# Optimization experiments

Measured on AMD Instinct MI355X. Metric: run time of the kernel, lower is better.

The kernel has to match this reference:

```python
import jax, jax.numpy as jnp
import numpy as np

N, E = 50000, 800000
IN, OUT, H, B = 512, 512, 8, 4  # num_bases=4, aggregators=['symnorm'] (PyG EGConv defaults)
FH = OUT // H  # per-head dim = 64
EPS = 1e-5


def setup_inputs() -> dict:
    key = jax.random.key(0)
    ks = jax.random.split(key, 8)
    s_in = 1.0 / np.sqrt(IN)
    return {
        "x": jax.random.normal(ks[0], (N, IN), jnp.float32),
        "edge_index": jax.random.randint(ks[1], (2, E), 0, N, jnp.int32),
        "W_bases": jax.random.normal(ks[2], (IN, B * FH), jnp.float32) * s_in,  # bases_lin (no bias)
        "W_comb": jax.random.normal(ks[3], (IN, H * B), jnp.float32) * s_in,    # comb_lin weight
        "b_comb": jnp.zeros((H * B,), jnp.float32),                               # comb_lin bias
        "conv_bias": jnp.zeros((OUT,), jnp.float32),                              # EGConv output bias
        "W_res": jax.random.normal(ks[4], (IN, OUT), jnp.float32) * s_in,        # res_connection
        "b_res": jnp.zeros((OUT,), jnp.float32),
        "gamma": jnp.ones((OUT,), jnp.float32),                                   # LayerNorm weight
        "beta": jnp.zeros((OUT,), jnp.float32),                                   # LayerNorm bias
    }


def reference(x, edge_index, W_bases, W_comb, b_comb, conv_bias, W_res, b_res, gamma, beta):
    n = x.shape[0]
    # --- gcn_norm with self-loops (symnorm aggregator) ---
    loops = jnp.arange(n, dtype=edge_index.dtype)
    src = jnp.concatenate([edge_index[0], loops])  # [E+N]
    dst = jnp.concatenate([edge_index[1], loops])
    deg = jax.ops.segment_sum(jnp.ones_like(src, dtype=x.dtype), dst, num_segments=n)
    dinv = jnp.where(deg > 0, jax.lax.rsqrt(jnp.maximum(deg, 1.0)), 0.0)
    norm = dinv[src] * dinv[dst]  # [E+N]

    # --- EGConv: bases projection, symnorm aggregation, per-head combination ---
    bases = x @ W_bases  # [N, B*FH]
    agg = jax.ops.segment_sum(bases[src] * norm[:, None], dst, num_segments=n)  # [N, B*FH]
    weightings = (x @ W_comb + b_comb).reshape(n, H, B)        # [N, H, B]  (num_aggrs=1)
    agg = agg.reshape(n, B, FH)                                  # [N, B, FH]
    conv_out = jnp.einsum('nhb,nbf->nhf', weightings, agg).reshape(n, OUT) + conv_bias

    # --- residual + LayerNorm + ReLU (dropout p=0 -> identity) ---
    out = conv_out + x @ W_res + b_res
    mu = out.mean(-1, keepdims=True)
    var = out.var(-1, keepdims=True)
    out = (out - mu) * jax.lax.rsqrt(var + EPS) * gamma + beta
    return jax.nn.relu(out)
```

## Files before the change

kernel.cpp:

```cpp
#include <hip/hip_runtime.h>
#include <hip/hip_bf16.h>

#define KDIM 512
#define ODIM 512
#define NB 4
#define NH 8
#define FH 64
#define BFH 256
#define HB 32
#define NCAT 896
#define COL_W 256
#define COL_R 288
#define LN_EPS 1e-5f
#define SCAN_BLK 1024

typedef __attribute__((ext_vector_type(8))) short short8;
typedef __attribute__((ext_vector_type(4))) float floatx4;

__device__ __forceinline__ float b2f(unsigned short u) {
    union { unsigned int i; float f; } v; v.i = ((unsigned int)u) << 16; return v.f;
}
__device__ __forceinline__ unsigned short f2b(float f) {
    __hip_bfloat16 h = __float2bfloat16(f);
    return *(unsigned short*)&h;
}
__device__ __forceinline__ void async16(const void* g, void* l) {
    __builtin_amdgcn_global_load_lds(
        (__attribute__((address_space(1))) unsigned int*)(g),
        (__attribute__((address_space(3))) unsigned int*)(l),
        16, 0, 0);
}

__global__ void deg_kernel(const int* __restrict__ dst, int* __restrict__ deg, int E) {
    int i = blockIdx.x * blockDim.x + threadIdx.x;
    if (i < E) atomicAdd(&deg[dst[i]], 1);
}

__global__ __launch_bounds__(256) void scan_sums_kernel(
        const int* __restrict__ deg, int* __restrict__ sums, int N) {
    int t = threadIdx.x;
    int idx = blockIdx.x * SCAN_BLK + t * 4;
    int4 v = {0, 0, 0, 0};
    if (idx + 3 < N) v = *(const int4*)(deg + idx);
    else {
        if (idx < N)     v.x = deg[idx];
        if (idx + 1 < N) v.y = deg[idx + 1];
        if (idx + 2 < N) v.z = deg[idx + 2];
        if (idx + 3 < N) v.w = deg[idx + 3];
    }
    int s = v.x + v.y + v.z + v.w;
    #pragma unroll
    for (int o = 32; o > 0; o >>= 1) s += __shfl_down(s, o, 64);
    __shared__ int ws[4];
    int lane = t & 63, w = t >> 6;
    if (lane == 0) ws[w] = s;
    __syncthreads();
    if (t == 0) sums[blockIdx.x] = ws[0] + ws[1] + ws[2] + ws[3];
}

__global__ __launch_bounds__(1024) void scan_base_kernel(
        int* __restrict__ sums, int nb) {
    __shared__ int sm[1024];
    int t = threadIdx.x;
    int own = (t < nb) ? sums[t] : 0;
    sm[t] = own;
    __syncthreads();
    for (int o = 1; o < 1024; o <<= 1) {
        int u = (t >= o) ? sm[t - o] : 0;
        __syncthreads();
        sm[t] += u;
        __syncthreads();
    }
    if (t < nb) sums[t] = sm[t] - own;
}

__global__ __launch_bounds__(256) void scan_write_kernel(
        const int* __restrict__ deg, const int* __restrict__ bases,
        int* __restrict__ offsets, int* __restrict__ woff,
        float* __restrict__ dinv, int N, int E) {
    int t = threadIdx.x;
    int idx = blockIdx.x * SCAN_BLK + t * 4;
    int4 v = {0, 0, 0, 0};
    if (idx + 3 < N) v = *(const int4*)(deg + idx);
    else {
        if (idx < N)     v.x = deg[idx];
        if (idx + 1 < N) v.y = deg[idx + 1];
        if (idx + 2 < N) v.z = deg[idx + 2];
        if (idx + 3 < N) v.w = deg[idx + 3];
    }
    int s = v.x + v.y + v.z + v.w;
    __shared__ int sm[256];
    sm[t] = s;
    __syncthreads();
    for (int o = 1; o < 256; o <<= 1) {
        int u = (t >= o) ? sm[t - o] : 0;
        __syncthreads();
        sm[t] += u;
        __syncthreads();
    }
    int o0 = sm[t] - s + bases[blockIdx.x];
    int o1 = o0 + v.x, o2 = o1 + v.y, o3 = o2 + v.z;
    if (idx + 3 < N) {
        int4 ov = {o0, o1, o2, o3};
        *(int4*)(offsets + idx) = ov;
        *(int4*)(woff + idx) = ov;
        float4 dv = {rsqrtf((float)v.x + 1.0f), rsqrtf((float)v.y + 1.0f),
                     rsqrtf((float)v.z + 1.0f), rsqrtf((float)v.w + 1.0f)};
        *(float4*)(dinv + idx) = dv;
    } else {
        int oo[4] = {o0, o1, o2, o3};
        int vv[4] = {v.x, v.y, v.z, v.w};
        for (int j = 0; j < 4; j++) {
            if (idx + j < N) {
                offsets[idx + j] = oo[j];
                woff[idx + j] = oo[j];
                dinv[idx + j] = rsqrtf((float)vv[j] + 1.0f);
            }
        }
    }
    if (blockIdx.x == 0 && t == 0) offsets[N] = E;
}

__global__ void fill_kernel(const int* __restrict__ src, const int* __restrict__ dst,
                            int* __restrict__ woff, int* __restrict__ ebuf, int E) {
    int i = blockIdx.x * blockDim.x + threadIdx.x;
    if (i < E) {
        int pos = atomicAdd(&woff[dst[i]], 1);
        ebuf[pos] = src[i];
    }
}

__global__ __launch_bounds__(256) void prep_kernel(
        const float* __restrict__ x, unsigned short* __restrict__ xb, long total4,
        int nCvtBlocks,
        const float* __restrict__ Wb, const float* __restrict__ Wc,
        const float* __restrict__ Wr, const float* __restrict__ bcomb,
        const float* __restrict__ bres,
        unsigned short* __restrict__ wT, float* __restrict__ bias_cat) {
    int blk = blockIdx.x;
    if (blk < nCvtBlocks) {
        long i = (long)blk * 256 + threadIdx.x;
        if (i >= total4) return;
        float4 v = ((const float4*)x)[i];
        ushort4 u;
        u.x = f2b(v.x); u.y = f2b(v.y); u.z = f2b(v.z); u.w = f2b(v.w);
        ((ushort4*)xb)[i] = u;
    } else {
        int idx = (blk - nCvtBlocks) * 256 + threadIdx.x;
        if (idx >= NCAT * KDIM) return;
        int c = idx >> 9, k = idx & (KDIM - 1);
        float v;
        if (c < BFH)                   v = Wb[(size_t)k * BFH + c];
        else if (c < COL_R)            v = Wc[(size_t)k * HB + (c - COL_W)];
        else if (c < COL_R + ODIM)     v = Wr[(size_t)k * ODIM + (c - COL_R)];
        else                           v = 0.0f;
        wT[(size_t)c * KDIM + k] = f2b(v);
        if (k == 0) {
            float bv = 0.0f;
            if (c >= COL_W && c < COL_R)             bv = bcomb[c - COL_W];
            else if (c >= COL_R && c < COL_R + ODIM) bv = bres[c - COL_R];
            bias_cat[c] = bv;
        }
    }
}

#define BM 128
#define BN 128
#define BK 32
#define SLD 136

__global__ __launch_bounds__(256) void mfma_gemm_kernel(
        const unsigned short* __restrict__ xb,
        const unsigned short* __restrict__ wT,
        const float* __restrict__ bias_cat,
        unsigned short* __restrict__ Cb,
        int N) {
    __shared__ short lds[16384];
    short* As0 = lds;
    short* Bs0 = lds + 4096;
    short* As1 = lds + 8192;
    short* Bs1 = lds + 12288;
    int t = threadIdx.x;
    int l = t & 63, w = t >> 6;
    int wr = w >> 1, wc = w & 1;
    int quad = l >> 4, m = l & 15;

    int nwg = gridDim.x;
    int orig = blockIdx.x;
    int q = nwg >> 3, r = nwg & 7;
    int xcd = orig & 7, slot = orig >> 3;
    int wg = (xcd < r) ? (xcd * (q + 1) + slot)
                       : (r * (q + 1) + (xcd - r) * q + slot);
    int bx = wg % 7, by = wg / 7;
    int row0 = by * BM;
    int col0 = bx * BN;

    floatx4 acc[4][4];
    floatx4 zero4 = {0.f, 0.f, 0.f, 0.f};
    #pragma unroll
    for (int i = 0; i < 4; i++)
        #pragma unroll
        for (int j = 0; j < 4; j++) acc[i][j] = zero4;

    int ar0 = row0 + (w << 4) + (l >> 2);
    int ar1 = ar0 + 64;
    int brow = col0 + (w << 4) + (l >> 2);
    int kk = (l & 3) * 8;
    const unsigned short* agp0 = xb + (size_t)min(ar0, N - 1) * KDIM + kk;
    const unsigned short* agp1 = xb + (size_t)min(ar1, N - 1) * KDIM + kk;
    const unsigned short* bgp0 = wT + (size_t)brow * KDIM + kk;
    const unsigned short* bgp1 = bgp0 + (size_t)64 * KDIM;

    auto stage = [&](short* A, short* B, int k0) {
        async16(agp0 + k0, A + w * 512);
        async16(agp1 + k0, A + 2048 + w * 512);
        async16(bgp0 + k0, B + w * 512);
        async16(bgp1 + k0, B + 2048 + w * 512);
    };
    auto compute = [&](const short* As, const short* Bs) {
        short8 a[4], b[4];
        #pragma unroll
        for (int i = 0; i < 4; i++)
            a[i] = *(const short8*)(As + (wr * 64 + i * 16 + m) * BK + quad * 8);
        #pragma unroll
        for (int j = 0; j < 4; j++)
            b[j] = *(const short8*)(Bs + (wc * 64 + j * 16 + m) * BK + quad * 8);
        #pragma unroll
        for (int i = 0; i < 4; i++)
            #pragma unroll
            for (int j = 0; j < 4; j++)
                acc[i][j] = __builtin_amdgcn_mfma_f32_16x16x32_bf16(
                    a[i], b[j], acc[i][j], 0, 0, 0);
    };

    stage(As0, Bs0, 0);
    __syncthreads();

    for (int k0 = 0; k0 < KDIM; k0 += 2 * BK) {
        if (k0 + BK < KDIM) stage(As1, Bs1, k0 + BK);
        compute(As0, Bs0);
        __syncthreads();
        if (k0 + 2 * BK < KDIM) stage(As0, Bs0, k0 + 2 * BK);
        compute(As1, Bs1);
        __syncthreads();
    }

    float bj[4];
    #pragma unroll
    for (int j = 0; j < 4; j++) bj[j] = bias_cat[col0 + wc * 64 + j * 16 + m];

    unsigned short* stage_buf = (unsigned short*)lds;
    #pragma unroll
    for (int i = 0; i < 4; i++) {
        __syncthreads();
        #pragma unroll
        for (int j = 0; j < 4; j++)
            #pragma unroll
            for (int r2 = 0; r2 < 4; r2++)
                stage_buf[(wr * 16 + quad * 4 + r2) * SLD + wc * 64 + j * 16 + m] =
                    f2b(acc[i][j][r2] + bj[j]);
        __syncthreads();
        #pragma unroll
        for (int u = t; u < 512; u += 256) {
            int lr = u >> 4, c8 = u & 15;
            int gr = row0 + ((lr & 16) ? 64 : 0) + i * 16 + (lr & 15);
            if (gr < N) {
                int4 v = *(const int4*)(stage_buf + lr * SLD + c8 * 8);
                *(int4*)(Cb + (size_t)gr * NCAT + col0 + c8 * 8) = v;
            }
        }
    }
}

__global__ __launch_bounds__(256) void gather_combine_kernel(
        const int* __restrict__ offsets, const int* __restrict__ ebuf,
        const float* __restrict__ dinv, const unsigned short* __restrict__ Cb,
        const float* __restrict__ conv_bias, const float* __restrict__ gamma,
        const float* __restrict__ beta, float* __restrict__ out, int N) {
    __shared__ float sagg[4][BFH];
    int wave = (blockIdx.x * blockDim.x + threadIdx.x) >> 6;
    int lane = threadIdx.x & 63;
    int wib = (threadIdx.x >> 6);
    if (wave >= N) return;
    int n = wave;
    float di = dinv[n];
    float self = di * di;
    ushort4 u = ((const ushort4*)(Cb + (size_t)n * NCAT))[lane];
    float ax = b2f(u.x) * self, ay = b2f(u.y) * self;
    float az = b2f(u.z) * self, aw = b2f(u.w) * self;
    int e = offsets[n], end = offsets[n + 1];
    int last = end - 1;
    for (; e < end; e += 8) {
        int s0, s1, s2, s3, s4, s5, s6, s7;
        float w0, w1, w2, w3, w4, w5, w6, w7;
        ushort4 u0, u1, u2, u3, u4, u5, u6, u7;
        s0 = ebuf[min(e + 0, last)];
        s1 = ebuf[min(e + 1, last)];
        s2 = ebuf[min(e + 2, last)];
        s3 = ebuf[min(e + 3, last)];
        s4 = ebuf[min(e + 4, last)];
        s5 = ebuf[min(e + 5, last)];
        s6 = ebuf[min(e + 6, last)];
        s7 = ebuf[min(e + 7, last)];
        w0 = (e + 0 < end) ? dinv[s0] * di : 0.0f;
        w1 = (e + 1 < end) ? dinv[s1] * di : 0.0f;
        w2 = (e + 2 < end) ? dinv[s2] * di : 0.0f;
        w3 = (e + 3 < end) ? dinv[s3] * di : 0.0f;
        w4 = (e + 4 < end) ? dinv[s4] * di : 0.0f;
        w5 = (e + 5 < end) ? dinv[s5] * di : 0.0f;
        w6 = (e + 6 < end) ? dinv[s6] * di : 0.0f;
        w7 = (e + 7 < end) ? dinv[s7] * di : 0.0f;
        u0 = ((const ushort4*)(Cb + (size_t)s0 * NCAT))[lane];
        u1 = ((const ushort4*)(Cb + (size_t)s1 * NCAT))[lane];
        u2 = ((const ushort4*)(Cb + (size_t)s2 * NCAT))[lane];
        u3 = ((const ushort4*)(Cb + (size_t)s3 * NCAT))[lane];
        u4 = ((const ushort4*)(Cb + (size_t)s4 * NCAT))[lane];
        u5 = ((const ushort4*)(Cb + (size_t)s5 * NCAT))[lane];
        u6 = ((const ushort4*)(Cb + (size_t)s6 * NCAT))[lane];
        u7 = ((const ushort4*)(Cb + (size_t)s7 * NCAT))[lane];
        ax += b2f(u0.x) * w0 + b2f(u1.x) * w1 + b2f(u2.x) * w2 + b2f(u3.x) * w3
            + b2f(u4.x) * w4 + b2f(u5.x) * w5 + b2f(u6.x) * w6 + b2f(u7.x) * w7;
        ay += b2f(u0.y) * w0 + b2f(u1.y) * w1 + b2f(u2.y) * w2 + b2f(u3.y) * w3
            + b2f(u4.y) * w4 + b2f(u5.y) * w5 + b2f(u6.y) * w6 + b2f(u7.y) * w7;
        az += b2f(u0.z) * w0 + b2f(u1.z) * w1 + b2f(u2.z) * w2 + b2f(u3.z) * w3
            + b2f(u4.z) * w4 + b2f(u5.z) * w5 + b2f(u6.z) * w6 + b2f(u7.z) * w7;
        aw += b2f(u0.w) * w0 + b2f(u1.w) * w1 + b2f(u2.w) * w2 + b2f(u3.w) * w3
            + b2f(u4.w) * w4 + b2f(u5.w) * w5 + b2f(u6.w) * w6 + b2f(u7.w) * w7;
    }
    float4 av = {ax, ay, az, aw};
    *(float4*)(&sagg[wib][lane * 4]) = av;

    int h = lane >> 3;
    int f0 = (lane & 7) * 8;
    int t0 = lane * 8;
    const unsigned short* crow = Cb + (size_t)n * NCAT;
    ushort4 wu = *(const ushort4*)(crow + COL_W + h * 4);
    float cw0 = b2f(wu.x), cw1 = b2f(wu.y), cw2 = b2f(wu.z), cw3 = b2f(wu.w);

    float4 b0a = *(const float4*)(&sagg[wib][0 * FH + f0]);
    float4 b0b = *(const float4*)(&sagg[wib][0 * FH + f0 + 4]);
    float4 b1a = *(const float4*)(&sagg[wib][1 * FH + f0]);
    float4 b1b = *(const float4*)(&sagg[wib][1 * FH + f0 + 4]);
    float4 b2a = *(const float4*)(&sagg[wib][2 * FH + f0]);
    float4 b2b = *(const float4*)(&sagg[wib][2 * FH + f0 + 4]);
    float4 b3a = *(const float4*)(&sagg[wib][3 * FH + f0]);
    float4 b3b = *(const float4*)(&sagg[wib][3 * FH + f0 + 4]);
    float a0[8] = {b0a.x, b0a.y, b0a.z, b0a.w, b0b.x, b0b.y, b0b.z, b0b.w};
    float a1[8] = {b1a.x, b1a.y, b1a.z, b1a.w, b1b.x, b1b.y, b1b.z, b1b.w};
    float a2[8] = {b2a.x, b2a.y, b2a.z, b2a.w, b2b.x, b2b.y, b2b.z, b2b.w};
    float a3[8] = {b3a.x, b3a.y, b3a.z, b3a.w, b3b.x, b3b.y, b3b.z, b3b.w};

    short8 rv = *(const short8*)(crow + COL_R + t0);
    float4 cb0 = *(const float4*)(conv_bias + t0);
    float4 cb1 = *(const float4*)(conv_bias + t0 + 4);
    float cb[8] = {cb0.x, cb0.y, cb0.z, cb0.w, cb1.x, cb1.y, cb1.z, cb1.w};

    float v[8];
    float s = 0.f, s2 = 0.f;
    #pragma unroll
    for (int j = 0; j < 8; j++) {
        float conv = cw0 * a0[j] + cw1 * a1[j] + cw2 * a2[j] + cw3 * a3[j];
        float val = conv + cb[j] + b2f((unsigned short)rv[j]);
        v[j] = val;
        s += val;
        s2 += val * val;
    }
    #pragma unroll
    for (int o = 32; o > 0; o >>= 1) {
        s  += __shfl_xor(s, o, 64);
        s2 += __shfl_xor(s2, o, 64);
    }
    float mu = s * (1.0f / (float)ODIM);
    float var = s2 * (1.0f / (float)ODIM) - mu * mu;
    float rstd = rsqrtf(var + LN_EPS);

    float4 g0 = *(const float4*)(gamma + t0);
    float4 g1 = *(const float4*)(gamma + t0 + 4);
    float4 be0 = *(const float4*)(beta + t0);
    float4 be1 = *(const float4*)(beta + t0 + 4);
    float g[8] = {g0.x, g0.y, g0.z, g0.w, g1.x, g1.y, g1.z, g1.w};
    float be[8] = {be0.x, be0.y, be0.z, be0.w, be1.x, be1.y, be1.z, be1.w};

    float ov[8];
    #pragma unroll
    for (int j = 0; j < 8; j++) {
        float o = (v[j] - mu) * rstd * g[j] + be[j];
        ov[j] = fmaxf(o, 0.0f);
    }
    float4* op = (float4*)(out + (size_t)n * ODIM + t0);
    op[0] = make_float4(ov[0], ov[1], ov[2], ov[3]);
    op[1] = make_float4(ov[4], ov[5], ov[6], ov[7]);
}

static inline char* ws_alloc(char*& p, size_t bytes) {
    char* r = p;
    p += (bytes + 255) & ~(size_t)255;
    return r;
}

extern "C" void kernel_launch(void* const* d_in, const int* in_sizes, int n_in,
                              void* d_out, int out_size, void* d_ws, size_t ws_size,
                              hipStream_t stream) {
    const float* x         = (const float*)d_in[0];
    const int*   ei        = (const int*)d_in[1];
    const float* W_bases   = (const float*)d_in[2];
    const float* W_comb    = (const float*)d_in[3];
    const float* b_comb    = (const float*)d_in[4];
    const float* conv_bias = (const float*)d_in[5];
    const float* W_res     = (const float*)d_in[6];
    const float* b_res     = (const float*)d_in[7];
    const float* gamma     = (const float*)d_in[8];
    const float* beta      = (const float*)d_in[9];

    int N = in_sizes[0] / KDIM;
    int E = in_sizes[1] / 2;
    const int* src = ei;
    const int* dst = ei + E;
    int nScanBlocks = (N + SCAN_BLK - 1) / SCAN_BLK;

    char* p = (char*)d_ws;
    int*   deg      = (int*)ws_alloc(p, sizeof(int) * (size_t)N);
    int*   offsets  = (int*)ws_alloc(p, sizeof(int) * (size_t)(N + 1));
    int*   woff     = (int*)ws_alloc(p, sizeof(int) * (size_t)N);
    int*   ebuf     = (int*)ws_alloc(p, sizeof(int) * (size_t)E);
    int*   sums     = (int*)ws_alloc(p, sizeof(int) * (size_t)nScanBlocks);
    float* dinv     = (float*)ws_alloc(p, sizeof(float) * (size_t)N);
    float* bias_cat = (float*)ws_alloc(p, sizeof(float) * NCAT);
    unsigned short* Cb  = (unsigned short*)ws_alloc(p, 2ull * N * NCAT);
    unsigned short* xb  = (unsigned short*)ws_alloc(p, 2ull * N * KDIM);
    unsigned short* wT  = (unsigned short*)ws_alloc(p, 2ull * NCAT * KDIM);
    float* out = (float*)d_out;

    hipMemsetAsync(deg, 0, sizeof(int) * (size_t)N, stream);

    long total4 = (long)N * KDIM / 4;
    int nCvtBlocks = (int)((total4 + 255) / 256);
    int nStageBlocks = (NCAT * KDIM + 255) / 256;
    prep_kernel<<<nCvtBlocks + nStageBlocks, 256, 0, stream>>>(
        x, xb, total4, nCvtBlocks, W_bases, W_comb, W_res, b_comb, b_res,
        wT, bias_cat);

    deg_kernel<<<(E + 255) / 256, 256, 0, stream>>>(dst, deg, E);
    scan_sums_kernel<<<nScanBlocks, 256, 0, stream>>>(deg, sums, N);
    scan_base_kernel<<<1, 1024, 0, stream>>>(sums, nScanBlocks);
    scan_write_kernel<<<nScanBlocks, 256, 0, stream>>>(deg, sums, offsets, woff,
                                                       dinv, N, E);
    fill_kernel<<<(E + 255) / 256, 256, 0, stream>>>(src, dst, woff, ebuf, E);

    int nYB = (N + BM - 1) / BM;
    mfma_gemm_kernel<<<7 * nYB, 256, 0, stream>>>(xb, wT, bias_cat, Cb, N);

    gather_combine_kernel<<<(N + 3) / 4, 256, 0, stream>>>(
        offsets, ebuf, dinv, Cb, conv_bias, gamma, beta, out, N);
}
```

Before: 423.5 us.

## Fuse degree count into prep, load GEMM B operand from global, split gather tail

The degree-counting atomics move into the prep kernel as extra blocks, which removes one kernel launch. The GEMM no longer stages the weight tile through LDS: each lane loads its B fragments straight from global memory, halving LDS use and dropping two async loads per stage. The gather loop gets an unclamped fast path for full groups of 8 edges and a separate masked tail. The direct global B loads are not shared across waves, which could raise L2 traffic and expose load latency inside the MFMA loop.

```diff
diff --git a/kernel.cpp b/kernel.cpp
--- a/kernel.cpp
+++ b/kernel.cpp
@@ -29,11 +29,6 @@
         (__attribute__((address_space(1))) unsigned int*)(g),
         (__attribute__((address_space(3))) unsigned int*)(l),
         16, 0, 0);
-}
-
-__global__ void deg_kernel(const int* __restrict__ dst, int* __restrict__ deg, int E) {
-    int i = blockIdx.x * blockDim.x + threadIdx.x;
-    if (i < E) atomicAdd(&deg[dst[i]], 1);
 }
 
 __global__ __launch_bounds__(256) void scan_sums_kernel(
@@ -132,11 +127,12 @@
 
 __global__ __launch_bounds__(256) void prep_kernel(
         const float* __restrict__ x, unsigned short* __restrict__ xb, long total4,
-        int nCvtBlocks,
+        int nCvtBlocks, int nStageBlocks,
         const float* __restrict__ Wb, const float* __restrict__ Wc,
         const float* __restrict__ Wr, const float* __restrict__ bcomb,
         const float* __restrict__ bres,
-        unsigned short* __restrict__ wT, float* __restrict__ bias_cat) {
+        unsigned short* __restrict__ wT, float* __restrict__ bias_cat,
+        const int* __restrict__ dst, int* __restrict__ deg, int E) {
     int blk = blockIdx.x;
     if (blk < nCvtBlocks) {
         long i = (long)blk * 256 + threadIdx.x;
@@ -145,7 +141,7 @@
         ushort4 u;
         u.x = f2b(v.x); u.y = f2b(v.y); u.z = f2b(v.z); u.w = f2b(v.w);
         ((ushort4*)xb)[i] = u;
-    } else {
+    } else if (blk < nCvtBlocks + nStageBlocks) {
         int idx = (blk - nCvtBlocks) * 256 + threadIdx.x;
         if (idx >= NCAT * KDIM) return;
         int c = idx >> 9, k = idx & (KDIM - 1);
@@ -161,6 +157,9 @@
             else if (c >= COL_R && c < COL_R + ODIM) bv = bres[c - COL_R];
             bias_cat[c] = bv;
         }
+    } else {
+        int i = (blk - nCvtBlocks - nStageBlocks) * 256 + threadIdx.x;
+        if (i < E) atomicAdd(&deg[dst[i]], 1);
     }
 }
 
@@ -175,11 +174,9 @@
         const float* __restrict__ bias_cat,
         unsigned short* __restrict__ Cb,
         int N) {
-    __shared__ short lds[16384];
+    __shared__ short lds[8192];
     short* As0 = lds;
-    short* Bs0 = lds + 4096;
-    short* As1 = lds + 8192;
-    short* Bs1 = lds + 12288;
+    short* As1 = lds + 4096;
     int t = threadIdx.x;
     int l = t & 63, w = t >> 6;
     int wr = w >> 1, wc = w & 1;
@@ -204,27 +201,26 @@
 
     int ar0 = row0 + (w << 4) + (l >> 2);
     int ar1 = ar0 + 64;
-    int brow = col0 + (w << 4) + (l >> 2);
     int kk = (l & 3) * 8;
     const unsigned short* agp0 = xb + (size_t)min(ar0, N - 1) * KDIM + kk;
     const unsigned short* agp1 = xb + (size_t)min(ar1, N - 1) * KDIM + kk;
-    const unsigned short* bgp0 = wT + (size_t)brow * KDIM + kk;
-    const unsigned short* bgp1 = bgp0 + (size_t)64 * KDIM;
-
-    auto stage = [&](short* A, short* B, int k0) {
+    const unsigned short* bq[4];
+    #pragma unroll
+    for (int j = 0; j < 4; j++)
+        bq[j] = wT + (size_t)(col0 + wc * 64 + j * 16 + m) * KDIM + quad * 8;
+
+    auto stage = [&](short* A, int k0) {
         async16(agp0 + k0, A + w * 512);
         async16(agp1 + k0, A + 2048 + w * 512);
-        async16(bgp0 + k0, B + w * 512);
-        async16(bgp1 + k0, B + 2048 + w * 512);
     };
-    auto compute = [&](const short* As, const short* Bs) {
+    auto compute = [&](const short* As, int k0) {
         short8 a[4], b[4];
+        #pragma unroll
+        for (int j = 0; j < 4; j++)
+            b[j] = *(const short8*)(bq[j] + k0);
         #pragma unroll
         for (int i = 0; i < 4; i++)
             a[i] = *(const short8*)(As + (wr * 64 + i * 16 + m) * BK + quad * 8);
-        #pragma unroll
-        for (int j = 0; j < 4; j++)
-            b[j] = *(const short8*)(Bs + (wc * 64 + j * 16 + m) * BK + quad * 8);
         #pragma unroll
         for (int i = 0; i < 4; i++)
             #pragma unroll
@@ -233,15 +229,15 @@
                     a[i], b[j], acc[i][j], 0, 0, 0);
     };
 
-    stage(As0, Bs0, 0);
+    stage(As0, 0);
     __syncthreads();
 
     for (int k0 = 0; k0 < KDIM; k0 += 2 * BK) {
-        if (k0 + BK < KDIM) stage(As1, Bs1, k0 + BK);
-        compute(As0, Bs0);
-        __syncthreads();
-        if (k0 + 2 * BK < KDIM) stage(As0, Bs0, k0 + 2 * BK);
-        compute(As1, Bs1);
+        if (k0 + BK < KDIM) stage(As1, k0 + BK);
+        compute(As0, k0);
+        __syncthreads();
+        if (k0 + 2 * BK < KDIM) stage(As0, k0 + 2 * BK);
+        compute(As1, k0 + BK);
         __syncthreads();
     }
 
@@ -289,35 +285,52 @@
     float ax = b2f(u.x) * self, ay = b2f(u.y) * self;
     float az = b2f(u.z) * self, aw = b2f(u.w) * self;
     int e = offsets[n], end = offsets[n + 1];
-    int last = end - 1;
-    for (; e < end; e += 8) {
-        int s0, s1, s2, s3, s4, s5, s6, s7;
-        float w0, w1, w2, w3, w4, w5, w6, w7;
-        ushort4 u0, u1, u2, u3, u4, u5, u6, u7;
-        s0 = ebuf[min(e + 0, last)];
-        s1 = ebuf[min(e + 1, last)];
-        s2 = ebuf[min(e + 2, last)];
-        s3 = ebuf[min(e + 3, last)];
-        s4 = ebuf[min(e + 4, last)];
-        s5 = ebuf[min(e + 5, last)];
-        s6 = ebuf[min(e + 6, last)];
-        s7 = ebuf[min(e + 7, last)];
-        w0 = (e + 0 < end) ? dinv[s0] * di : 0.0f;
-        w1 = (e + 1 < end) ? dinv[s1] * di : 0.0f;
-        w2 = (e + 2 < end) ? dinv[s2] * di : 0.0f;
-        w3 = (e + 3 < end) ? dinv[s3] * di : 0.0f;
-        w4 = (e + 4 < end) ? dinv[s4] * di : 0.0f;
-        w5 = (e + 5 < end) ? dinv[s5] * di : 0.0f;
-        w6 = (e + 6 < end) ? dinv[s6] * di : 0.0f;
-        w7 = (e + 7 < end) ? dinv[s7] * di : 0.0f;
-        u0 = ((const ushort4*)(Cb + (size_t)s0 * NCAT))[lane];
-        u1 = ((const ushort4*)(Cb + (size_t)s1 * NCAT))[lane];
-        u2 = ((const ushort4*)(Cb + (size_t)s2 * NCAT))[lane];
-        u3 = ((const ushort4*)(Cb + (size_t)s3 * NCAT))[lane];
-        u4 = ((const ushort4*)(Cb + (size_t)s4 * NCAT))[lane];
-        u5 = ((const ushort4*)(Cb + (size_t)s5 * NCAT))[lane];
-        u6 = ((const ushort4*)(Cb + (size_t)s6 * NCAT))[lane];
-        u7 = ((const ushort4*)(Cb + (size_t)s7 * NCAT))[lane];
+    for (; e + 8 <= end; e += 8) {
+        int s0 = ebuf[e + 0], s1 = ebuf[e + 1], s2 = ebuf[e + 2], s3 = ebuf[e + 3];
+        int s4 = ebuf[e + 4], s5 = ebuf[e + 5], s6 = ebuf[e + 6], s7 = ebuf[e + 7];
+        float w0 = dinv[s0] * di, w1 = dinv[s1] * di;
+        float w2 = dinv[s2] * di, w3 = dinv[s3] * di;
+        float w4 = dinv[s4] * di, w5 = dinv[s5] * di;
+        float w6 = dinv[s6] * di, w7 = dinv[s7] * di;
+        ushort4 u0 = ((const ushort4*)(Cb + (size_t)s0 * NCAT))[lane];
+        ushort4 u1 = ((const ushort4*)(Cb + (size_t)s1 * NCAT))[lane];
+        ushort4 u2 = ((const ushort4*)(Cb + (size_t)s2 * NCAT))[lane];
+        ushort4 u3 = ((const ushort4*)(Cb + (size_t)s3 * NCAT))[lane];
+        ushort4 u4 = ((const ushort4*)(Cb + (size_t)s4 * NCAT))[lane];
+        ushort4 u5 = ((const ushort4*)(Cb + (size_t)s5 * NCAT))[lane];
+        ushort4 u6 = ((const ushort4*)(Cb + (size_t)s6 * NCAT))[lane];
+        ushort4 u7 = ((const ushort4*)(Cb + (size_t)s7 * NCAT))[lane];
+        ax += b2f(u0.x) * w0 + b2f(u1.x) * w1 + b2f(u2.x) * w2 + b2f(u3.x) * w3
+            + b2f(u4.x) * w4 + b2f(u5.x) * w5 + b2f(u6.x) * w6 + b2f(u7.x) * w7;
+        ay += b2f(u0.y) * w0 + b2f(u1.y) * w1 + b2f(u2.y) * w2 + b2f(u3.y) * w3
+            + b2f(u4.y) * w4 + b2f(u5.y) * w5 + b2f(u6.y) * w6 + b2f(u7.y) * w7;
+        az += b2f(u0.z) * w0 + b2f(u1.z) * w1 + b2f(u2.z) * w2 + b2f(u3.z) * w3
+            + b2f(u4.z) * w4 + b2f(u5.z) * w5 + b2f(u6.z) * w6 + b2f(u7.z) * w7;
+        aw += b2f(u0.w) * w0 + b2f(u1.w) * w1 + b2f(u2.w) * w2 + b2f(u3.w) * w3
+            + b2f(u4.w) * w4 + b2f(u5.w) * w5 + b2f(u6.w) * w6 + b2f(u7.w) * w7;
+    }
+    if (e < end) {
+        int last = end - 1;
+        int s0 = ebuf[min(e + 0, last)], s1 = ebuf[min(e + 1, last)];
+        int s2 = ebuf[min(e + 2, last)], s3 = ebuf[min(e + 3, last)];
+        int s4 = ebuf[min(e + 4, last)], s5 = ebuf[min(e + 5, last)];
+        int s6 = ebuf[min(e + 6, last)], s7 = ebuf[min(e + 7, last)];
+        float w0 = (e + 0 < end) ? dinv[s0] * di : 0.0f;
+        float w1 = (e + 1 < end) ? dinv[s1] * di : 0.0f;
+        float w2 = (e + 2 < end) ? dinv[s2] * di : 0.0f;
+        float w3 = (e + 3 < end) ? dinv[s3] * di : 0.0f;
+        float w4 = (e + 4 < end) ? dinv[s4] * di : 0.0f;
+        float w5 = (e + 5 < end) ? dinv[s5] * di : 0.0f;
+        float w6 = (e + 6 < end) ? dinv[s6] * di : 0.0f;
+        float w7 = (e + 7 < end) ? dinv[s7] * di : 0.0f;
+        ushort4 u0 = ((const ushort4*)(Cb + (size_t)s0 * NCAT))[lane];
+        ushort4 u1 = ((const ushort4*)(Cb + (size_t)s1 * NCAT))[lane];
+        ushort4 u2 = ((const ushort4*)(Cb + (size_t)s2 * NCAT))[lane];
+        ushort4 u3 = ((const ushort4*)(Cb + (size_t)s3 * NCAT))[lane];
+        ushort4 u4 = ((const ushort4*)(Cb + (size_t)s4 * NCAT))[lane];
+        ushort4 u5 = ((const ushort4*)(Cb + (size_t)s5 * NCAT))[lane];
+        ushort4 u6 = ((const ushort4*)(Cb + (size_t)s6 * NCAT))[lane];
+        ushort4 u7 = ((const ushort4*)(Cb + (size_t)s7 * NCAT))[lane];
         ax += b2f(u0.x) * w0 + b2f(u1.x) * w1 + b2f(u2.x) * w2 + b2f(u3.x) * w3
             + b2f(u4.x) * w4 + b2f(u5.x) * w5 + b2f(u6.x) * w6 + b2f(u7.x) * w7;
         ay += b2f(u0.y) * w0 + b2f(u1.y) * w1 + b2f(u2.y) * w2 + b2f(u3.y) * w3
@@ -436,11 +449,11 @@
     long total4 = (long)N * KDIM / 4;
     int nCvtBlocks = (int)((total4 + 255) / 256);
     int nStageBlocks = (NCAT * KDIM + 255) / 256;
-    prep_kernel<<<nCvtBlocks + nStageBlocks, 256, 0, stream>>>(
-        x, xb, total4, nCvtBlocks, W_bases, W_comb, W_res, b_comb, b_res,
-        wT, bias_cat);
-
-    deg_kernel<<<(E + 255) / 256, 256, 0, stream>>>(dst, deg, E);
+    int nDegBlocks = (E + 255) / 256;
+    prep_kernel<<<nCvtBlocks + nStageBlocks + nDegBlocks, 256, 0, stream>>>(
+        x, xb, total4, nCvtBlocks, nStageBlocks, W_bases, W_comb, W_res,
+        b_comb, b_res, wT, bias_cat, dst, deg, E);
+
     scan_sums_kernel<<<nScanBlocks, 256, 0, stream>>>(deg, sums, N);
     scan_base_kernel<<<1, 1024, 0, stream>>>(sums, nScanBlocks);
     scan_write_kernel<<<nScanBlocks, 256, 0, stream>>>(deg, sums, offsets, woff,
```

Result: slower. 457.4 us (+8.0%).
